# Optimization experiments

Measured on AMD Instinct MI355X. Metric: run time of the kernel, lower is better.

Reference implementation:

```python
import jax, jax.numpy as jnp
import numpy as np

N, E, D, S, H, L = 20000, 320000, 128, 16, 4, 64


def _ln(x, g, b):
    m = x.mean(-1, keepdims=True)
    v = jnp.mean((x - m) ** 2, -1, keepdims=True)
    return (x - m) / jnp.sqrt(v + 1e-6) * g + b


def _mlp3(x, w1, b1, g1, be1, w2, b2, g2, be2, w3, b3):
    h = jax.nn.silu(_ln(x @ w1 + b1, g1, be1))
    h = jax.nn.silu(_ln(h @ w2 + b2, g2, be2))
    return h @ w3 + b3


def _seg_softmax(a, idx, n):
    # torch_geometric.utils.softmax: per-destination-group stable softmax
    m = jax.ops.segment_max(a, idx, num_segments=n)
    m = jnp.where(jnp.isfinite(m), m, 0.0)
    e = jnp.exp(a - m[idx])
    s = jax.ops.segment_sum(e, idx, num_segments=n)
    return e / (s[idx] + 1e-16)


def setup_inputs() -> dict:
    key = jax.random.key(0)
    ks = jax.random.split(key, 32)
    rn = lambda k, sh, sc=1.0: jax.random.normal(k, sh, dtype=jnp.float32) * sc
    li = lambda k, fi, fo: rn(k, (fi, fo), 1.0 / np.sqrt(fi))
    z = lambda n_: jnp.zeros((n_,), jnp.float32)
    o = lambda n_: jnp.ones((n_,), jnp.float32)
    inp = {
        'node_in': rn(ks[0], (N, D)),
        'node_embed': rn(ks[1], (N, D)),
        'edge_sh': rn(ks[2], (E, S)),
        'edge_length_embedding': rn(ks[3], (E, L)),
        'edge_src': jax.random.randint(ks[4], (E,), 0, N, dtype=jnp.int32),
        'edge_dst': jax.random.randint(ks[5], (E,), 0, N, dtype=jnp.int32),
        'batch': jnp.zeros((N,), jnp.int32),
        'pre_lin_w': li(ks[6], 2 * D + L, D),
        'tp2_w1': li(ks[7], L, 64), 'tp2_b1': z(64),
        'tp2_w2': li(ks[8], 64, H * S), 'tp2_b2': z(H * S),
        'a_w1': li(ks[9], L, 64), 'a_b1': z(64), 'a_g1': o(64), 'a_be1': z(64),
        'a_w2': li(ks[10], 64, 64), 'a_b2': z(64), 'a_g2': o(64), 'a_be2': z(64),
        'a_w3': li(ks[11], 64, H), 'a_b3': z(H),
        'lin_w': li(ks[12], D * H, D),
        'lin_edge_w': li(ks[13], D * H, 64),
        's_w1': li(ks[14], 64, 64), 's_b1': z(64), 's_g1': o(64), 's_be1': z(64),
        's_w2': li(ks[15], 64, 64), 's_b2': z(64), 's_g2': o(64), 's_be2': z(64),
        's_w3': li(ks[16], 64, 32), 's_b3': z(32),
    }
    return inp


def reference(node_in, node_embed, edge_sh, edge_length_embedding, edge_src, edge_dst, batch,
              pre_lin_w, tp2_w1, tp2_b1, tp2_w2, tp2_b2,
              a_w1, a_b1, a_g1, a_be1, a_w2, a_b2, a_g2, a_be2, a_w3, a_b3,
              lin_w, lin_edge_w,
              s_w1, s_b1, s_g1, s_be1, s_w2, s_b2, s_g2, s_be2, s_w3, s_b3):
    e = edge_length_embedding.shape[0]
    n = node_in.shape[0]
    # gather + pre_lin
    msg = jnp.concatenate([node_in[edge_src], node_in[edge_dst], edge_length_embedding], -1) @ pre_lin_w  # [E,D]
    # EquiConv tp2: channelwise TP with radial-MLP per-edge per-(head,sh) weights
    radial = jax.nn.silu(edge_length_embedding @ tp2_w1 + tp2_b1) @ tp2_w2 + tp2_b2  # [E,H*S]
    scal = jnp.einsum('ehs,es->eh', radial.reshape(e, H, S), edge_sh)  # [E,H]
    value = msg[:, None, :] * scal[:, :, None]  # [E,H,D]
    alpha = _mlp3(edge_length_embedding, a_w1, a_b1, a_g1, a_be1, a_w2, a_b2, a_g2, a_be2, a_w3, a_b3)  # [E,H]
    edge_out = value * alpha[:, :, None]  # [E,H,D]
    edge_scalar = _mlp3(edge_out.reshape(e, -1) @ lin_edge_w,
                        s_w1, s_b1, s_g1, s_be1, s_w2, s_b2, s_g2, s_be2, s_w3, s_b3)  # [E,32]
    asm = _seg_softmax(alpha, edge_dst, n)  # [E,H]
    node_fea = jax.ops.segment_sum(value * asm[:, :, None], edge_dst, num_segments=n)  # [N,H,D]
    node_out = node_fea.reshape(n, -1) @ lin_w  # [N,D]
    return node_out, edge_scalar
```

## Files before the change

kernel.cpp:

```cpp
#include <hip/hip_runtime.h>

#define NN 20000
#define EE 320000
#define WTOT 27648
#define P3N (EE*64/8 + NN*128/8)

typedef unsigned short u16;
typedef unsigned int u32;
typedef __attribute__((ext_vector_type(8))) short bf16x8;
typedef __attribute__((ext_vector_type(8))) _Float16 f16x8;
typedef __attribute__((ext_vector_type(4))) float f32x4;

__device__ __forceinline__ float bf2f(u16 u){
  union { u32 i; float f; } v; v.i = ((u32)u) << 16; return v.f;
}
__device__ __forceinline__ u16 f2bf(float f){
  union { float f; u32 i; } v; v.f = f;
  u32 i = v.i;
  return (u16)((i + 0x7FFFu + ((i >> 16) & 1u)) >> 16);
}
__device__ __forceinline__ u16 f2h(float f){
  union { _Float16 h[2]; u32 u; } v; v.h[0] = (_Float16)f;
  return (u16)(v.u & 0xFFFF);
}
__device__ __forceinline__ float h2f(u16 u){
  union { u32 i; _Float16 h[2]; } v; v.i = u; return (float)v.h[0];
}
__device__ __forceinline__ u32 packh2(float a, float b){
  return ((u32)f2h(b) << 16) | (u32)f2h(a);
}
__device__ __forceinline__ float fsilu(float y){
  return y * __builtin_amdgcn_rcpf(1.f + __expf(-y));
}

__global__ __launch_bounds__(256) void k_prep_all(
    const float* __restrict__ elen, const float* __restrict__ node_in,
    u16* __restrict__ elen16, u16* __restrict__ node16,
    int* __restrict__ counts,
    const float* __restrict__ plw, const float* __restrict__ lew,
    const float* __restrict__ lw,
    u16* __restrict__ Bt1, u16* __restrict__ Bt2, u16* __restrict__ Bt3,
    const float* __restrict__ aw1, const float* __restrict__ aw2, const float* __restrict__ aw3,
    const float* __restrict__ rw1, const float* __restrict__ rw2,
    const float* __restrict__ sw1, const float* __restrict__ sw2, const float* __restrict__ sw3,
    u16* __restrict__ W)
{
  size_t gi = (size_t)blockIdx.x * 256 + threadIdx.x;
  if (gi < (size_t)P3N) {
    const size_t n1 = (size_t)EE * 64 / 8;
    const float* src;
    u16* dst;
    if (gi < n1) { src = elen + gi*8; dst = elen16 + gi*8; }
    else { size_t j = gi - n1; src = node_in + j*8; dst = node16 + j*8; }
    float4 a = ((const float4*)src)[0];
    float4 b = ((const float4*)src)[1];
    uint4 vh;
    vh.x = packh2(a.x, a.y); vh.y = packh2(a.z, a.w);
    vh.z = packh2(b.x, b.y); vh.w = packh2(b.z, b.w);
    *(uint4*)dst = vh;
    return;
  }
  long j = (long)gi - P3N;
  if (j < NN) { counts[j] = 0; return; }
  j -= NN;
  if (j < 128*320) {
    int n = (int)j / 320, k = (int)j % 320;
    Bt1[j] = f2h(plw[k*128 + n]);
    return;
  }
  j -= 128*320;
  if (j < 256*128) {
    int n = (int)j / 128, k = (int)j % 128;
    int h = n >> 6, c = n & 63;
    Bt2[j] = f2h(lew[(h*128 + k)*64 + c]);
    return;
  }
  j -= 256*128;
  if (j < 128*512) {
    int n = (int)j / 512, k = (int)j % 512;
    Bt3[j] = f2bf(lw[k*128 + n]);
    return;
  }
  j -= 128*512;
  if (j < WTOT) {
    float v = 0.f;
    long i = j;
    if (i < 8192)      { int n = i >> 6, k = i & 63;
                         v = (n < 64) ? aw1[k*64 + n] : rw1[k*64 + (n - 64)]; }
    else if ((i -= 8192) < 4096) { int n = i >> 6, k = i & 63; v = aw2[k*64 + n]; }
    else if ((i -= 4096) < 1024) { int n = i >> 6, k = i & 63; v = (n < 4) ? aw3[k*4 + n] : 0.f; }
    else if ((i -= 1024) < 4096) { int n = i >> 6, k = i & 63; v = rw2[k*64 + n]; }
    else if ((i -= 4096) < 4096) { int n = i >> 6, k = i & 63; v = sw1[k*64 + n]; }
    else if ((i -= 4096) < 4096) { int n = i >> 6, k = i & 63; v = sw2[k*64 + n]; }
    else               { i -= 4096; int n = i >> 6, k = i & 63; v = sw3[k*32 + n]; }
    W[j] = f2h(v);
  }
}

__global__ __launch_bounds__(256) void k_count(const int* __restrict__ edst, int* __restrict__ counts){
  int e = blockIdx.x * 256 + threadIdx.x;
  if (e < EE) atomicAdd(&counts[edst[e]], 1);
}
__global__ __launch_bounds__(1024) void k_scan(const int* __restrict__ counts,
                                               int* __restrict__ offs, int* __restrict__ cursor){
  __shared__ int part[1024];
  int t = threadIdx.x;
  int c0 = t * 20, c1 = c0 + 20; if (c1 > NN) c1 = NN; if (c0 > NN) c0 = NN;
  int s = 0;
  for (int i = c0; i < c1; ++i) s += counts[i];
  part[t] = s;
  __syncthreads();
  int acc = s;
  #pragma unroll
  for (int d = 1; d < 1024; d <<= 1) {
    int v = (t >= d) ? part[t - d] : 0;
    __syncthreads();
    acc += v;
    part[t] = acc;
    __syncthreads();
  }
  if (t == 1023) offs[NN] = acc;
  int run = acc - s;
  for (int i = c0; i < c1; ++i) { offs[i] = run; cursor[i] = run; run += counts[i]; }
}
__global__ __launch_bounds__(256) void k_fill(const int* __restrict__ edst,
                                              int* __restrict__ cursor, int* __restrict__ eids){
  int e = blockIdx.x * 256 + threadIdx.x;
  if (e < EE) { int p = atomicAdd(&cursor[edst[e]], 1); eids[p] = e; }
}
__global__ __launch_bounds__(256) void k_sort2(const int* __restrict__ offs, int* __restrict__ eids){
  int w = threadIdx.x >> 6, lane = threadIdx.x & 63;
  int n = blockIdx.x * 4 + w;
  if (n >= NN) return;
  int beg = offs[n], end = offs[n+1], deg = end - beg;
  if (deg <= 1) return;
  if (deg <= 64) {
    int v = (lane < deg) ? eids[beg + lane] : 0x7fffffff;
    int rank = 0;
    for (int j = 0; j < deg; ++j) {
      int u = __shfl(v, j);
      rank += (u < v) ? 1 : 0;
    }
    if (lane < deg) eids[beg + rank] = v;
  } else if (lane == 0) {
    for (int i = beg + 1; i < end; ++i) {
      int v = eids[i]; int j = i - 1;
      while (j >= beg && eids[j] > v) { eids[j+1] = eids[j]; --j; }
      eids[j+1] = v;
    }
  }
}

template<int NI>
__device__ __forceinline__ void gemm16_lds(const u16 (*X)[72], int wrow, int lane,
                                           const u16* __restrict__ B, f32x4 acc[2][4])
{
  const int fr = lane & 15, fc = lane >> 4;
  #pragma unroll
  for (int mi = 0; mi < 2; ++mi)
    #pragma unroll
    for (int ni = 0; ni < NI; ++ni)
      acc[mi][ni] = (f32x4){0.f, 0.f, 0.f, 0.f};
  #pragma unroll
  for (int kk = 0; kk < 2; ++kk) {
    f16x8 a0 = *(const f16x8*)&X[wrow + fr][kk*32 + fc*8];
    f16x8 a1 = *(const f16x8*)&X[wrow + 16 + fr][kk*32 + fc*8];
    #pragma unroll
    for (int ni = 0; ni < NI; ++ni) {
      f16x8 b = *(const f16x8*)(B + (size_t)(ni*16 + fr)*64 + kk*32 + fc*8);
      acc[0][ni] = __builtin_amdgcn_mfma_f32_16x16x32_f16(a0, b, acc[0][ni], 0, 0, 0);
      acc[1][ni] = __builtin_amdgcn_mfma_f32_16x16x32_f16(a1, b, acc[1][ni], 0, 0, 0);
    }
  }
}

template<int NI>
__device__ __forceinline__ void gemm16_lds1(const u16 (*X)[72], int wrow, int lane,
                                            const u16* __restrict__ B, f32x4 acc[4])
{
  const int fr = lane & 15, fc = lane >> 4;
  #pragma unroll
  for (int ni = 0; ni < NI; ++ni) acc[ni] = (f32x4){0.f, 0.f, 0.f, 0.f};
  #pragma unroll
  for (int kk = 0; kk < 2; ++kk) {
    f16x8 a = *(const f16x8*)&X[wrow + fr][kk*32 + fc*8];
    #pragma unroll
    for (int ni = 0; ni < NI; ++ni) {
      f16x8 b = *(const f16x8*)(B + (size_t)(ni*16 + fr)*64 + kk*32 + fc*8);
      acc[ni] = __builtin_amdgcn_mfma_f32_16x16x32_f16(a, b, acc[ni], 0, 0, 0);
    }
  }
}

__device__ __forceinline__ void gemm16_glb8(const u16* __restrict__ X, int row0, int lane,
                                            const u16* __restrict__ B, f32x4 acc[2][8])
{
  const int fr = lane & 15, fc = lane >> 4;
  #pragma unroll
  for (int mi = 0; mi < 2; ++mi)
    #pragma unroll
    for (int ni = 0; ni < 8; ++ni)
      acc[mi][ni] = (f32x4){0.f, 0.f, 0.f, 0.f};
  #pragma unroll
  for (int kk = 0; kk < 2; ++kk) {
    f16x8 a0 = *(const f16x8*)(X + (size_t)(row0 + fr)*64 + kk*32 + fc*8);
    f16x8 a1 = *(const f16x8*)(X + (size_t)(row0 + 16 + fr)*64 + kk*32 + fc*8);
    #pragma unroll
    for (int ni = 0; ni < 8; ++ni) {
      f16x8 b = *(const f16x8*)(B + (size_t)(ni*16 + fr)*64 + kk*32 + fc*8);
      acc[0][ni] = __builtin_amdgcn_mfma_f32_16x16x32_f16(a0, b, acc[0][ni], 0, 0, 0);
      acc[1][ni] = __builtin_amdgcn_mfma_f32_16x16x32_f16(a1, b, acc[1][ni], 0, 0, 0);
    }
  }
}

template<bool LN>
__device__ __forceinline__ void act_store16(f32x4 acc[2][4],
    const float* __restrict__ b, const float* __restrict__ g, const float* __restrict__ be,
    u16 (*H)[72], int wrow, int lane)
{
  const int fr = lane & 15, fc = lane >> 4;
  float bv[4], gv[4], bev[4];
  #pragma unroll
  for (int ni = 0; ni < 4; ++ni) {
    bv[ni] = b[ni*16 + fr];
    if (LN) { gv[ni] = g[ni*16 + fr]; bev[ni] = be[ni*16 + fr]; }
  }
  #pragma unroll
  for (int mi = 0; mi < 2; ++mi)
    #pragma unroll
    for (int j = 0; j < 4; ++j) {
      int r = wrow + mi*16 + fc*4 + j;
      float x[4];
      #pragma unroll
      for (int ni = 0; ni < 4; ++ni) x[ni] = acc[mi][ni][j] + bv[ni];
      if (LN) {
        float s  = x[0] + x[1] + x[2] + x[3];
        float s2 = x[0]*x[0] + x[1]*x[1] + x[2]*x[2] + x[3]*x[3];
        #pragma unroll
        for (int off = 1; off < 16; off <<= 1) {
          s  += __shfl_xor(s,  off);
          s2 += __shfl_xor(s2, off);
        }
        float mu  = s * (1.f/64.f);
        float var = s2 * (1.f/64.f) - mu*mu;
        float rs  = rsqrtf(var + 1e-6f);
        #pragma unroll
        for (int ni = 0; ni < 4; ++ni) x[ni] = (x[ni] - mu)*rs*gv[ni] + bev[ni];
      }
      #pragma unroll
      for (int ni = 0; ni < 4; ++ni)
        H[r][ni*16 + fr] = f2h(fsilu(x[ni]));
    }
}

template<bool LN>
__device__ __forceinline__ void act_store16_1(f32x4 acc[4],
    const float* __restrict__ b, const float* __restrict__ g, const float* __restrict__ be,
    u16 (*H)[72], int wrow, int lane)
{
  const int fr = lane & 15, fc = lane >> 4;
  float bv[4], gv[4], bev[4];
  #pragma unroll
  for (int ni = 0; ni < 4; ++ni) {
    bv[ni] = b[ni*16 + fr];
    if (LN) { gv[ni] = g[ni*16 + fr]; bev[ni] = be[ni*16 + fr]; }
  }
  #pragma unroll
  for (int j = 0; j < 4; ++j) {
    int r = wrow + fc*4 + j;
    float x[4];
    #pragma unroll
    for (int ni = 0; ni < 4; ++ni) x[ni] = acc[ni][j] + bv[ni];
    if (LN) {
      float s  = x[0] + x[1] + x[2] + x[3];
      float s2 = x[0]*x[0] + x[1]*x[1] + x[2]*x[2] + x[3]*x[3];
      #pragma unroll
      for (int off = 1; off < 16; off <<= 1) {
        s  += __shfl_xor(s,  off);
        s2 += __shfl_xor(s2, off);
      }
      float mu  = s * (1.f/64.f);
      float var = s2 * (1.f/64.f) - mu*mu;
      float rs  = rsqrtf(var + 1e-6f);
      #pragma unroll
      for (int ni = 0; ni < 4; ++ni) x[ni] = (x[ni] - mu)*rs*gv[ni] + bev[ni];
    }
    #pragma unroll
    for (int ni = 0; ni < 4; ++ni)
      H[r][ni*16 + fr] = f2h(fsilu(x[ni]));
  }
}

union ESmem {
  struct { u16 Ha[128][72]; u16 Hr[128][72]; } m;
  struct { u16 Bs[2][128][40]; } g;
};
__global__ __launch_bounds__(256, 4) void k_edge1(
  const u16* __restrict__ elen16, const float* __restrict__ esh,
  const u16* __restrict__ Wm,
  const float* __restrict__ ab1, const float* __restrict__ ag1, const float* __restrict__ abe1,
  const float* __restrict__ ab2, const float* __restrict__ ag2, const float* __restrict__ abe2,
  const float* __restrict__ ab3,
  const float* __restrict__ tb1, const float* __restrict__ tb2,
  float* __restrict__ ealpha_g, float* __restrict__ scal_g, float* __restrict__ cbuf_g,
  const u16* __restrict__ node16,
  const int* __restrict__ esrc, const int* __restrict__ edst,
  const u16* __restrict__ Bt1, u16* __restrict__ msgb)
{
  __shared__ ESmem u;
  __shared__ float aS[128][4];
  const u16* Wc1 = Wm;
  const u16* Wa2 = Wm + 8192;
  const u16* Wa3 = Wm + 12288;
  const u16* Wr2 = Wm + 13312;
  const int tid = threadIdx.x;
  const int wave = tid >> 6, lane = tid & 63;
  const int fr = lane & 15, fc = lane >> 4;
  const int wrow = wave * 32;
  const int e0 = blockIdx.x * 128;
  {
    {
      f32x4 acc8[2][8];
      gemm16_glb8(elen16, e0 + wrow, lane, Wc1, acc8);
      float bva[4], gva[4], beva[4], bvr[4];
      #pragma unroll
      for (int ni = 0; ni < 4; ++ni) {
        bva[ni] = ab1[ni*16 + fr]; gva[ni] = ag1[ni*16 + fr]; beva[ni] = abe1[ni*16 + fr];
        bvr[ni] = tb1[ni*16 + fr];
      }
      #pragma unroll
      for (int mi = 0; mi < 2; ++mi)
        #pragma unroll
        for (int j = 0; j < 4; ++j) {
          int r = wrow + mi*16 + fc*4 + j;
          float xa[4], xr[4];
          #pragma unroll
          for (int ni = 0; ni < 4; ++ni) {
            xa[ni] = acc8[mi][ni][j] + bva[ni];
            xr[ni] = acc8[mi][ni+4][j] + bvr[ni];
          }
          float s  = xa[0] + xa[1] + xa[2] + xa[3];
          float s2 = xa[0]*xa[0] + xa[1]*xa[1] + xa[2]*xa[2] + xa[3]*xa[3];
          #pragma unroll
          for (int off = 1; off < 16; off <<= 1) {
            s  += __shfl_xor(s,  off);
            s2 += __shfl_xor(s2, off);
          }
          float mu  = s * (1.f/64.f);
          float var = s2 * (1.f/64.f) - mu*mu;
          float rs  = rsqrtf(var + 1e-6f);
          #pragma unroll
          for (int ni = 0; ni < 4; ++ni) {
            float y = (xa[ni] - mu)*rs*gva[ni] + beva[ni];
            u.m.Ha[r][ni*16 + fr] = f2h(fsilu(y));
            u.m.Hr[r][ni*16 + fr] = f2h(fsilu(xr[ni]));
          }
        }
    }
    f32x4 acc[2][4];
    gemm16_lds<4>(u.m.Ha, wrow, lane, Wa2, acc);
    act_store16<true>(acc, ab2, ag2, abe2, u.m.Ha, wrow, lane);
    gemm16_lds<1>(u.m.Ha, wrow, lane, Wa3, acc);
    {
      float bv = (fr < 4) ? ab3[fr] : 0.f;
      #pragma unroll
      for (int mi = 0; mi < 2; ++mi)
        #pragma unroll
        for (int j = 0; j < 4; ++j) {
          int r = wrow + mi*16 + fc*4 + j;
          float v = acc[mi][0][j] + bv;
          if (fr < 4) {
            ealpha_g[(size_t)(e0 + r)*4 + fr] = __expf(v);
            aS[r][fr] = v;
          }
        }
    }
    gemm16_lds<4>(u.m.Hr, wrow, lane, Wr2, acc);
    {
      float bv[4];
      #pragma unroll
      for (int ni = 0; ni < 4; ++ni) bv[ni] = tb2[ni*16 + fr];
      #pragma unroll
      for (int mi = 0; mi < 2; ++mi)
        #pragma unroll
        for (int j = 0; j < 4; ++j) {
          int r = wrow + mi*16 + fc*4 + j;
          float shv = esh[(size_t)(e0 + r)*16 + fr];
          float sc[4];
          #pragma unroll
          for (int ni = 0; ni < 4; ++ni) {
            float t = (acc[mi][ni][j] + bv[ni]) * shv;
            #pragma unroll
            for (int off = 1; off < 16; off <<= 1) t += __shfl_xor(t, off);
            sc[ni] = t;
          }
          if (fr == 0) {
            float4 sv; sv.x = sc[0]; sv.y = sc[1]; sv.z = sc[2]; sv.w = sc[3];
            *(float4*)(scal_g + (size_t)(e0 + r)*4) = sv;
            float4 cv;
            cv.x = sc[0]*aS[r][0]; cv.y = sc[1]*aS[r][1];
            cv.z = sc[2]*aS[r][2]; cv.w = sc[3]*aS[r][3];
            *(float4*)(cbuf_g + (size_t)(e0 + r)*4) = cv;
          }
        }
    }
  }
  __syncthreads();
  {
    const int r0 = e0 + wrow + fr;
    const int r1 = r0 + 16;
    const int s0 = esrc[r0], d0 = edst[r0];
    const int s1 = esrc[r1], d1 = edst[r1];
    const int sr = tid >> 1, sh = tid & 1;
    const u16* bstg = Bt1 + (size_t)sr*320 + sh*16;
    {
      const uint4* bp = (const uint4*)(bstg);
      *(uint4*)&u.g.Bs[0][sr][sh*16]     = bp[0];
      *(uint4*)&u.g.Bs[0][sr][sh*16 + 8] = bp[1];
    }
    f32x4 acc[2][8];
    #pragma unroll
    for (int mi = 0; mi < 2; ++mi)
      #pragma unroll
      for (int ni = 0; ni < 8; ++ni)
        acc[mi][ni] = (f32x4){0.f, 0.f, 0.f, 0.f};
    __syncthreads();
    #pragma unroll
    for (int k0i = 0; k0i < 10; ++k0i) {
      const int buf = k0i & 1;
      if (k0i + 1 < 10) {
        const uint4* bp = (const uint4*)(bstg + (k0i + 1)*32);
        *(uint4*)&u.g.Bs[buf^1][sr][sh*16]     = bp[0];
        *(uint4*)&u.g.Bs[buf^1][sr][sh*16 + 8] = bp[1];
      }
      const int k0 = k0i * 32;
      const u16 *ap0, *ap1;
      if (k0 < 128)      { ap0 = node16 + (size_t)s0*128 + k0;
                           ap1 = node16 + (size_t)s1*128 + k0; }
      else if (k0 < 256) { ap0 = node16 + (size_t)d0*128 + (k0 - 128);
                           ap1 = node16 + (size_t)d1*128 + (k0 - 128); }
      else               { ap0 = elen16 + (size_t)r0*64 + (k0 - 256);
                           ap1 = elen16 + (size_t)r1*64 + (k0 - 256); }
      f16x8 a0 = *(const f16x8*)(ap0 + fc*8);
      f16x8 a1 = *(const f16x8*)(ap1 + fc*8);
      #pragma unroll
      for (int ni = 0; ni < 8; ++ni) {
        f16x8 b = *(const f16x8*)&u.g.Bs[buf][ni*16 + fr][fc*8];
        acc[0][ni] = __builtin_amdgcn_mfma_f32_16x16x32_f16(a0, b, acc[0][ni], 0, 0, 0);
        acc[1][ni] = __builtin_amdgcn_mfma_f32_16x16x32_f16(a1, b, acc[1][ni], 0, 0, 0);
      }
      __syncthreads();
    }
    #pragma unroll
    for (int mi = 0; mi < 2; ++mi)
      #pragma unroll
      for (int j = 0; j < 4; ++j) {
        int row = wrow + mi*16 + fc*4 + j;
        size_t base = (size_t)(e0 + row)*128 + fr;
        #pragma unroll
        for (int ni = 0; ni < 8; ++ni)
          msgb[base + ni*16] = f2h(acc[mi][ni][j]);
      }
  }
}

__global__ __launch_bounds__(256, 4) void g2s(
    const u16* __restrict__ msgb, const u16* __restrict__ Bt2,
    const float* __restrict__ cbuf, const u16* __restrict__ Wm,
    const float* __restrict__ b1, const float* __restrict__ g1, const float* __restrict__ be1,
    const float* __restrict__ b2, const float* __restrict__ g2, const float* __restrict__ be2,
    const float* __restrict__ b3,
    float* __restrict__ oute)
{
  __shared__ u16 Bs[256][40];
  __shared__ u16 X[64][72];
  __shared__ float cS[64][4];
  const u16* Ws1 = Wm + 17408;
  const u16* Ws2 = Wm + 21504;
  const u16* Ws3 = Wm + 25600;
  const int tid = threadIdx.x, wave = tid >> 6, lane = tid & 63;
  const int e0 = blockIdx.x * 64;
  const int fr = lane & 15, fc = lane >> 4;
  const int wrow = wave * 16;
  cS[tid >> 2][tid & 3] = cbuf[(size_t)e0*4 + tid];
  f16x8 a[4];
  {
    const u16* arow = msgb + (size_t)(e0 + wrow + fr)*128 + fc*8;
    #pragma unroll
    for (int k0i = 0; k0i < 4; ++k0i) a[k0i] = *(const f16x8*)(arow + k0i*32);
  }
  f32x4 acc[16];
  #pragma unroll
  for (int ni = 0; ni < 16; ++ni) acc[ni] = (f32x4){0.f, 0.f, 0.f, 0.f};
  const u16* bsrc = Bt2 + (size_t)tid*128;
  #pragma unroll
  for (int k0i = 0; k0i < 4; ++k0i) {
    {
      const uint4* bp = (const uint4*)(bsrc + k0i*32);
      *(uint4*)&Bs[tid][0]  = bp[0];
      *(uint4*)&Bs[tid][8]  = bp[1];
      *(uint4*)&Bs[tid][16] = bp[2];
      *(uint4*)&Bs[tid][24] = bp[3];
    }
    __syncthreads();
    #pragma unroll
    for (int ni = 0; ni < 16; ++ni) {
      f16x8 b = *(const f16x8*)&Bs[ni*16 + fr][fc*8];
      acc[ni] = __builtin_amdgcn_mfma_f32_16x16x32_f16(a[k0i], b, acc[ni], 0, 0, 0);
    }
    __syncthreads();
  }
  #pragma unroll
  for (int j = 0; j < 4; ++j) {
    int r = wrow + fc*4 + j;
    float c0 = cS[r][0], c1 = cS[r][1], c2 = cS[r][2], c3 = cS[r][3];
    #pragma unroll
    for (int m = 0; m < 4; ++m) {
      float y = c0*acc[m][j] + c1*acc[4+m][j] + c2*acc[8+m][j] + c3*acc[12+m][j];
      X[r][m*16 + fr] = f2h(y);
    }
  }
  f32x4 sa[4];
  gemm16_lds1<4>(X, wrow, lane, Ws1, sa);
  act_store16_1<true>(sa, b1, g1, be1, X, wrow, lane);
  gemm16_lds1<4>(X, wrow, lane, Ws2, sa);
  act_store16_1<true>(sa, b2, g2, be2, X, wrow, lane);
  gemm16_lds1<2>(X, wrow, lane, Ws3, sa);
  {
    float bv0 = b3[fr], bv1 = b3[16 + fr];
    #pragma unroll
    for (int j = 0; j < 4; ++j) {
      int r = wrow + fc*4 + j;
      oute[(size_t)(e0 + r)*32 + fr]      = sa[0][j] + bv0;
      oute[(size_t)(e0 + r)*32 + 16 + fr] = sa[1][j] + bv1;
    }
  }
}

__global__ __launch_bounds__(256) void k_node(
  const int* __restrict__ offs, const int* __restrict__ eids,
  const float* __restrict__ ealpha, const float* __restrict__ scal,
  const u16* __restrict__ msgb, u16* __restrict__ nfb)
{
  const int w = threadIdx.x >> 6, lane = threadIdx.x & 63;
  const int n = blockIdx.x * 4 + w;
  const int beg = offs[n], end = offs[n+1];
  float se0=0.f, se1=0.f, se2=0.f, se3=0.f;
  float f00=0.f, f01=0.f, f10=0.f, f11=0.f, f20=0.f, f21=0.f, f30=0.f, f31=0.f;
  for (int i = beg; i < end; ++i) {
    int eid = eids[i];
    float4 a = *(const float4*)(ealpha + (size_t)eid*4);
    float4 s = *(const float4*)(scal + (size_t)eid*4);
    se0 += a.x; se1 += a.y; se2 += a.z; se3 += a.w;
    float w0 = a.x*s.x, w1 = a.y*s.y, w2 = a.z*s.z, w3 = a.w*s.w;
    float v0 = h2f(msgb[(size_t)eid*128 + lane]);
    float v1 = h2f(msgb[(size_t)eid*128 + 64 + lane]);
    f00 = fmaf(w0, v0, f00); f01 = fmaf(w0, v1, f01);
    f10 = fmaf(w1, v0, f10); f11 = fmaf(w1, v1, f11);
    f20 = fmaf(w2, v0, f20); f21 = fmaf(w2, v1, f21);
    f30 = fmaf(w3, v0, f30); f31 = fmaf(w3, v1, f31);
  }
  float i0 = 1.f/(se0 + 1e-16f), i1 = 1.f/(se1 + 1e-16f);
  float i2 = 1.f/(se2 + 1e-16f), i3 = 1.f/(se3 + 1e-16f);
  size_t b = (size_t)n * 512;
  nfb[b + 0*128 + lane]      = f2bf(f00*i0);
  nfb[b + 0*128 + 64 + lane] = f2bf(f01*i0);
  nfb[b + 1*128 + lane]      = f2bf(f10*i1);
  nfb[b + 1*128 + 64 + lane] = f2bf(f11*i1);
  nfb[b + 2*128 + lane]      = f2bf(f20*i2);
  nfb[b + 2*128 + 64 + lane] = f2bf(f21*i2);
  nfb[b + 3*128 + lane]      = f2bf(f30*i3);
  nfb[b + 3*128 + 64 + lane] = f2bf(f31*i3);
}

__global__ __launch_bounds__(256) void g10_out(
    const u16* __restrict__ nfb, const u16* __restrict__ Bt3,
    float* __restrict__ out)
{
  __shared__ u16 As[128][40];
  __shared__ u16 Bs[128][40];
  const int tid = threadIdx.x;
  const int n0 = blockIdx.x * 128;
  const int wave = tid >> 6, lane = tid & 63;
  const int wr = (wave >> 1) * 64, wc = (wave & 1) * 64;
  const int fr = lane & 15, fc = lane >> 4;
  f32x4 acc[4][4] = {};
  const int r = tid >> 1, half = tid & 1;
  const int n = n0 + r;
  for (int k0 = 0; k0 < 512; k0 += 32) {
    uint4 z; z.x=0; z.y=0; z.z=0; z.w=0;
    uint4 v0 = z, v1 = z;
    if (n < NN) {
      const uint4* apv = (const uint4*)(nfb + (size_t)n*512 + k0 + half*16);
      v0 = apv[0]; v1 = apv[1];
    }
    *(uint4*)&As[r][half*16]     = v0;
    *(uint4*)&As[r][half*16 + 8] = v1;
    const uint4* bp = (const uint4*)(Bt3 + (size_t)r*512 + k0 + half*16);
    *(uint4*)&Bs[r][half*16]     = bp[0];
    *(uint4*)&Bs[r][half*16 + 8] = bp[1];
    __syncthreads();
    bf16x8 a[4], b[4];
    #pragma unroll
    for (int mi = 0; mi < 4; ++mi) a[mi] = *(const bf16x8*)&As[wr + mi*16 + fr][fc*8];
    #pragma unroll
    for (int ni = 0; ni < 4; ++ni) b[ni] = *(const bf16x8*)&Bs[wc + ni*16 + fr][fc*8];
    #pragma unroll
    for (int mi = 0; mi < 4; ++mi)
      #pragma unroll
      for (int ni = 0; ni < 4; ++ni)
        acc[mi][ni] = __builtin_amdgcn_mfma_f32_16x16x32_bf16(a[mi], b[ni], acc[mi][ni], 0, 0, 0);
    __syncthreads();
  }
  #pragma unroll
  for (int mi = 0; mi < 4; ++mi)
    #pragma unroll
    for (int j = 0; j < 4; ++j) {
      int rowg = n0 + wr + mi*16 + fc*4 + j;
      if (rowg < NN) {
        size_t base = (size_t)rowg*128 + wc + fr;
        #pragma unroll
        for (int ni = 0; ni < 4; ++ni)
          out[base + ni*16] = acc[mi][ni][j];
      }
    }
}

extern "C" void kernel_launch(void* const* d_in, const int* in_sizes, int n_in,
                              void* d_out, int out_size, void* d_ws, size_t ws_size,
                              hipStream_t stream)
{
  const float* node_in    = (const float*)d_in[0];
  const float* edge_sh    = (const float*)d_in[2];
  const float* elen       = (const float*)d_in[3];
  const int*   esrc       = (const int*)d_in[4];
  const int*   edst       = (const int*)d_in[5];
  const float* pre_lin_w  = (const float*)d_in[7];
  const float* tp2_w1     = (const float*)d_in[8];
  const float* tp2_b1     = (const float*)d_in[9];
  const float* tp2_w2     = (const float*)d_in[10];
  const float* tp2_b2     = (const float*)d_in[11];
  const float* a_w1  = (const float*)d_in[12];
  const float* a_b1  = (const float*)d_in[13];
  const float* a_g1  = (const float*)d_in[14];
  const float* a_be1 = (const float*)d_in[15];
  const float* a_w2  = (const float*)d_in[16];
  const float* a_b2  = (const float*)d_in[17];
  const float* a_g2  = (const float*)d_in[18];
  const float* a_be2 = (const float*)d_in[19];
  const float* a_w3  = (const float*)d_in[20];
  const float* a_b3  = (const float*)d_in[21];
  const float* lin_w      = (const float*)d_in[22];
  const float* lin_edge_w = (const float*)d_in[23];
  const float* s_w1  = (const float*)d_in[24];
  const float* s_b1  = (const float*)d_in[25];
  const float* s_g1  = (const float*)d_in[26];
  const float* s_be1 = (const float*)d_in[27];
  const float* s_w2  = (const float*)d_in[28];
  const float* s_b2  = (const float*)d_in[29];
  const float* s_g2  = (const float*)d_in[30];
  const float* s_be2 = (const float*)d_in[31];
  const float* s_w3  = (const float*)d_in[32];
  const float* s_b3  = (const float*)d_in[33];

  float* out_node = (float*)d_out;
  float* out_edge = out_node + (size_t)NN * 128;

  char* ws = (char*)d_ws;
  size_t off = 0;
  auto take = [&](size_t bytes) -> char* {
    char* p = ws + off;
    off = (off + bytes + 255) & ~(size_t)255;
    return p;
  };
  u16*   msgb   = (u16*)take((size_t)EE * 128 * 2);
  u16*   elen16 = (u16*)take((size_t)EE * 64 * 2);
  u16*   node16 = (u16*)take((size_t)NN * 128 * 2);
  u16*   nfb    = (u16*)take((size_t)NN * 512 * 2);
  float* ealpha = (float*)take((size_t)EE * 4 * 4);
  float* scal   = (float*)take((size_t)EE * 4 * 4);
  float* cbuf   = (float*)take((size_t)EE * 4 * 4);
  int*   counts = (int*)take((size_t)NN * 4);
  int*   offs   = (int*)take((size_t)(NN + 1) * 4);
  int*   cursor = (int*)take((size_t)NN * 4);
  int*   eids   = (int*)take((size_t)EE * 4);
  u16*   Bt1    = (u16*)take((size_t)128 * 320 * 2);
  u16*   Bt2    = (u16*)take((size_t)256 * 128 * 2);
  u16*   Bt3    = (u16*)take((size_t)128 * 512 * 2);
  u16*   Wmlp   = (u16*)take((size_t)WTOT * 2);

  const long prep_total = (long)P3N + NN + 128*320 + 256*128 + 128*512 + WTOT;
  k_prep_all<<<(int)((prep_total + 255)/256), 256, 0, stream>>>(
      elen, node_in, elen16, node16, counts,
      pre_lin_w, lin_edge_w, lin_w, Bt1, Bt2, Bt3,
      a_w1, a_w2, a_w3, tp2_w1, tp2_w2, s_w1, s_w2, s_w3, Wmlp);
  k_count<<<EE/256, 256, 0, stream>>>(edst, counts);
  k_scan<<<1, 1024, 0, stream>>>(counts, offs, cursor);
  k_fill<<<EE/256, 256, 0, stream>>>(edst, cursor, eids);
  k_sort2<<<NN/4, 256, 0, stream>>>(offs, eids);
  k_edge1<<<EE/128, 256, 0, stream>>>(elen16, edge_sh, Wmlp,
                                      a_b1, a_g1, a_be1, a_b2, a_g2, a_be2, a_b3,
                                      tp2_b1, tp2_b2, ealpha, scal, cbuf,
                                      node16, esrc, edst, Bt1, msgb);
  g2s<<<EE/64, 256, 0, stream>>>(msgb, Bt2, cbuf, Wmlp,
                                 s_b1, s_g1, s_be1, s_b2, s_g2, s_be2, s_b3, out_edge);
  k_node<<<NN/4, 256, 0, stream>>>(offs, eids, ealpha, scal, msgb, nfb);
  g10_out<<<(NN + 127)/128, 256, 0, stream>>>(nfb, Bt3, out_node);
}
```

Measured before the change: 396.0 us.

## Precompute per-node pre_lin projections and gather them per edge

The pre_lin matmul is split by linearity. The node_in[src] and node_in[dst] parts are computed once per node in a new kernel (N×128 → N×256), instead of once per edge over K=256. The edge kernel now runs only the K=64 edge-length part, stages the result in LDS, and adds the gathered per-node projections from the new buffer in fp16. This removes most of the per-edge MFMA work in exchange for an extra kernel, an extra N×256 buffer, and fp16 rounding of the partial sums before they are added.

Result: no change. 403.0 us (+1.8%).

```diff
diff --git a/kernel.cpp b/kernel.cpp
--- a/kernel.cpp
+++ b/kernel.cpp
@@ -151,6 +151,61 @@
   }
 }
 
+__global__ __launch_bounds__(256, 4) void k_na(
+    const u16* __restrict__ node16, const u16* __restrict__ Bt1, u16* __restrict__ na)
+{
+  __shared__ u16 Bsa[128][40], Bsb[128][40];
+  const int tid = threadIdx.x, wave = tid >> 6, lane = tid & 63;
+  const int fr = lane & 15, fc = lane >> 4;
+  const int wrow = wave * 16;
+  const int n0 = blockIdx.x * 64;
+  int arow_i = n0 + wrow + fr; if (arow_i >= NN) arow_i = NN - 1;
+  f16x8 a[4];
+  {
+    const u16* arow = node16 + (size_t)arow_i*128 + fc*8;
+    #pragma unroll
+    for (int k0i = 0; k0i < 4; ++k0i) a[k0i] = *(const f16x8*)(arow + k0i*32);
+  }
+  f32x4 acc1[8], acc2[8];
+  #pragma unroll
+  for (int ni = 0; ni < 8; ++ni) {
+    acc1[ni] = (f32x4){0.f, 0.f, 0.f, 0.f};
+    acc2[ni] = (f32x4){0.f, 0.f, 0.f, 0.f};
+  }
+  const int srow = tid & 127, swhich = tid >> 7;
+  #pragma unroll
+  for (int k0i = 0; k0i < 4; ++k0i) {
+    {
+      const uint4* bp = (const uint4*)(Bt1 + (size_t)srow*320 + swhich*128 + k0i*32);
+      u16 (*dstp)[40] = swhich ? Bsb : Bsa;
+      *(uint4*)&dstp[srow][0]  = bp[0];
+      *(uint4*)&dstp[srow][8]  = bp[1];
+      *(uint4*)&dstp[srow][16] = bp[2];
+      *(uint4*)&dstp[srow][24] = bp[3];
+    }
+    __syncthreads();
+    #pragma unroll
+    for (int ni = 0; ni < 8; ++ni) {
+      f16x8 b1 = *(const f16x8*)&Bsa[ni*16 + fr][fc*8];
+      f16x8 b2 = *(const f16x8*)&Bsb[ni*16 + fr][fc*8];
+      acc1[ni] = __builtin_amdgcn_mfma_f32_16x16x32_f16(a[k0i], b1, acc1[ni], 0, 0, 0);
+      acc2[ni] = __builtin_amdgcn_mfma_f32_16x16x32_f16(a[k0i], b2, acc2[ni], 0, 0, 0);
+    }
+    __syncthreads();
+  }
+  #pragma unroll
+  for (int j = 0; j < 4; ++j) {
+    int n = n0 + wrow + fc*4 + j;
+    if (n < NN) {
+      #pragma unroll
+      for (int ni = 0; ni < 8; ++ni) {
+        na[(size_t)n*256 + ni*16 + fr]       = f2h(acc1[ni][j]);
+        na[(size_t)n*256 + 128 + ni*16 + fr] = f2h(acc2[ni][j]);
+      }
+    }
+  }
+}
+
 template<int NI>
 __device__ __forceinline__ void gemm16_lds(const u16 (*X)[72], int wrow, int lane,
                                            const u16* __restrict__ B, f32x4 acc[2][4])
@@ -294,7 +349,8 @@
 
 union ESmem {
   struct { u16 Ha[128][72]; u16 Hr[128][72]; } m;
-  struct { u16 Bs[2][128][40]; } g;
+  u16 Bs[128][40];
+  u16 M[128][136];
 };
 __global__ __launch_bounds__(256, 4) void k_edge1(
   const u16* __restrict__ elen16, const float* __restrict__ esh,
@@ -304,7 +360,7 @@
   const float* __restrict__ ab3,
   const float* __restrict__ tb1, const float* __restrict__ tb2,
   float* __restrict__ ealpha_g, float* __restrict__ scal_g, float* __restrict__ cbuf_g,
-  const u16* __restrict__ node16,
+  const u16* __restrict__ na,
   const int* __restrict__ esrc, const int* __restrict__ edst,
   const u16* __restrict__ Bt1, u16* __restrict__ msgb)
 {
@@ -410,43 +466,26 @@
   {
     const int r0 = e0 + wrow + fr;
     const int r1 = r0 + 16;
-    const int s0 = esrc[r0], d0 = edst[r0];
-    const int s1 = esrc[r1], d1 = edst[r1];
     const int sr = tid >> 1, sh = tid & 1;
-    const u16* bstg = Bt1 + (size_t)sr*320 + sh*16;
-    {
-      const uint4* bp = (const uint4*)(bstg);
-      *(uint4*)&u.g.Bs[0][sr][sh*16]     = bp[0];
-      *(uint4*)&u.g.Bs[0][sr][sh*16 + 8] = bp[1];
-    }
     f32x4 acc[2][8];
     #pragma unroll
     for (int mi = 0; mi < 2; ++mi)
       #pragma unroll
       for (int ni = 0; ni < 8; ++ni)
         acc[mi][ni] = (f32x4){0.f, 0.f, 0.f, 0.f};
-    __syncthreads();
-    #pragma unroll
-    for (int k0i = 0; k0i < 10; ++k0i) {
-      const int buf = k0i & 1;
-      if (k0i + 1 < 10) {
-        const uint4* bp = (const uint4*)(bstg + (k0i + 1)*32);
-        *(uint4*)&u.g.Bs[buf^1][sr][sh*16]     = bp[0];
-        *(uint4*)&u.g.Bs[buf^1][sr][sh*16 + 8] = bp[1];
-      }
-      const int k0 = k0i * 32;
-      const u16 *ap0, *ap1;
-      if (k0 < 128)      { ap0 = node16 + (size_t)s0*128 + k0;
-                           ap1 = node16 + (size_t)s1*128 + k0; }
-      else if (k0 < 256) { ap0 = node16 + (size_t)d0*128 + (k0 - 128);
-                           ap1 = node16 + (size_t)d1*128 + (k0 - 128); }
-      else               { ap0 = elen16 + (size_t)r0*64 + (k0 - 256);
-                           ap1 = elen16 + (size_t)r1*64 + (k0 - 256); }
-      f16x8 a0 = *(const f16x8*)(ap0 + fc*8);
-      f16x8 a1 = *(const f16x8*)(ap1 + fc*8);
+    #pragma unroll
+    for (int k0i = 0; k0i < 2; ++k0i) {
+      {
+        const uint4* bp = (const uint4*)(Bt1 + (size_t)sr*320 + 256 + k0i*32 + sh*16);
+        *(uint4*)&u.Bs[sr][sh*16]     = bp[0];
+        *(uint4*)&u.Bs[sr][sh*16 + 8] = bp[1];
+      }
+      __syncthreads();
+      f16x8 a0 = *(const f16x8*)(elen16 + (size_t)r0*64 + k0i*32 + fc*8);
+      f16x8 a1 = *(const f16x8*)(elen16 + (size_t)r1*64 + k0i*32 + fc*8);
       #pragma unroll
       for (int ni = 0; ni < 8; ++ni) {
-        f16x8 b = *(const f16x8*)&u.g.Bs[buf][ni*16 + fr][fc*8];
+        f16x8 b = *(const f16x8*)&u.Bs[ni*16 + fr][fc*8];
         acc[0][ni] = __builtin_amdgcn_mfma_f32_16x16x32_f16(a0, b, acc[0][ni], 0, 0, 0);
         acc[1][ni] = __builtin_amdgcn_mfma_f32_16x16x32_f16(a1, b, acc[1][ni], 0, 0, 0);
       }
@@ -457,11 +496,27 @@
       #pragma unroll
       for (int j = 0; j < 4; ++j) {
         int row = wrow + mi*16 + fc*4 + j;
-        size_t base = (size_t)(e0 + row)*128 + fr;
         #pragma unroll
         for (int ni = 0; ni < 8; ++ni)
-          msgb[base + ni*16] = f2h(acc[mi][ni][j]);
-      }
+          u.M[row][ni*16 + fr] = f2h(acc[mi][ni][j]);
+      }
+    __syncthreads();
+    {
+      const int r = tid >> 1, half = tid & 1;
+      const int e = e0 + r;
+      const int s_r = esrc[e], d_r = edst[e];
+      const u16* pa1 = na + (size_t)s_r*256 + half*64;
+      const u16* pa2 = na + (size_t)d_r*256 + 128 + half*64;
+      u16* dst = msgb + (size_t)e*128 + half*64;
+      #pragma unroll
+      for (int q = 0; q < 8; ++q) {
+        f16x8 mv = *(const f16x8*)&u.M[r][half*64 + q*8];
+        f16x8 v1 = *(const f16x8*)(pa1 + q*8);
+        f16x8 v2 = *(const f16x8*)(pa2 + q*8);
+        f16x8 sm = mv + v1 + v2;
+        *(f16x8*)(dst + q*8) = sm;
+      }
+    }
   }
 }
 
@@ -677,6 +732,7 @@
   u16*   msgb   = (u16*)take((size_t)EE * 128 * 2);
   u16*   elen16 = (u16*)take((size_t)EE * 64 * 2);
   u16*   node16 = (u16*)take((size_t)NN * 128 * 2);
+  u16*   na     = (u16*)take((size_t)NN * 256 * 2);
   u16*   nfb    = (u16*)take((size_t)NN * 512 * 2);
   float* ealpha = (float*)take((size_t)EE * 4 * 4);
   float* scal   = (float*)take((size_t)EE * 4 * 4);
@@ -695,6 +751,7 @@
       elen, node_in, elen16, node16, counts,
       pre_lin_w, lin_edge_w, lin_w, Bt1, Bt2, Bt3,
       a_w1, a_w2, a_w3, tp2_w1, tp2_w2, s_w1, s_w2, s_w3, Wmlp);
+  k_na<<<(NN + 63)/64, 256, 0, stream>>>(node16, Bt1, na);
   k_count<<<EE/256, 256, 0, stream>>>(edst, counts);
   k_scan<<<1, 1024, 0, stream>>>(counts, offs, cursor);
   k_fill<<<EE/256, 256, 0, stream>>>(edst, cursor, eids);
@@ -702,7 +759,7 @@
   k_edge1<<<EE/128, 256, 0, stream>>>(elen16, edge_sh, Wmlp,
                                       a_b1, a_g1, a_be1, a_b2, a_g2, a_be2, a_b3,
                                       tp2_b1, tp2_b2, ealpha, scal, cbuf,
-                                      node16, esrc, edst, Bt1, msgb);
+                                      na, esrc, edst, Bt1, msgb);
   g2s<<<EE/64, 256, 0, stream>>>(msgb, Bt2, cbuf, Wmlp,
                                  s_b1, s_g1, s_be1, s_b2, s_g2, s_be2, s_b3, out_edge);
   k_node<<<NN/4, 256, 0, stream>>>(offs, eids, ealpha, scal, msgb, nfb);
```
